# Kernel tuning notes

Measured on AMD Instinct MI355X. Metric: run time of the kernel, lower is better.

The kernel has to match this reference:

```python
import jax, jax.numpy as jnp
import numpy as np

EPS = 1e-5  # BatchNorm2d default eps


def conv1x1_bn(x, w, g, b, m, v):
    # 1x1 conv (no bias) + inference BatchNorm folded to scale/shift
    y = jnp.einsum('bchw,oc->bohw', x, w)
    s = g / jnp.sqrt(v + EPS)
    return y * s[None, :, None, None] + (b - m * s)[None, :, None, None]


def setup_inputs() -> dict:
    key = jax.random.key(0)
    ks = jax.random.split(key, 18)
    B, C, H, W = 4, 256, 64, 64
    KD, NH = 16, 8
    DH = KD * NH
    f = jax.random.normal
    u = jax.random.uniform
    return {
        'x': f(ks[0], (B, C, H, W), jnp.float32),
        'key_v_input_reduction': f(ks[1], (1,), jnp.float32),
        'w_qk': f(ks[2], (KD, C), jnp.float32) * 0.05,
        'g_qk': u(ks[3], (KD,), jnp.float32, 0.5, 1.5),
        'b_qk': f(ks[4], (KD,), jnp.float32) * 0.05,
        'm_qk': f(ks[5], (KD,), jnp.float32) * 0.05,
        'v_qk': u(ks[6], (KD,), jnp.float32, 0.5, 1.5),
        'w_v': f(ks[7], (DH, C), jnp.float32) * 0.05,
        'g_v': u(ks[8], (DH,), jnp.float32, 0.5, 1.5),
        'b_v': f(ks[9], (DH,), jnp.float32) * 0.05,
        'm_v': f(ks[10], (DH,), jnp.float32) * 0.05,
        'v_v': u(ks[11], (DH,), jnp.float32, 0.5, 1.5),
        'w_p': f(ks[12], (C, DH), jnp.float32) * 0.05,
        'g_p': u(ks[13], (C,), jnp.float32, 0.5, 1.5),
        'b_p': f(ks[14], (C,), jnp.float32) * 0.05,
        'm_p': f(ks[15], (C,), jnp.float32) * 0.05,
        'v_p': u(ks[16], (C,), jnp.float32, 0.5, 1.5),
    }


def reference(x, key_v_input_reduction, w_qk, g_qk, b_qk, m_qk, v_qk,
              w_v, g_v, b_v, m_v, v_v, w_p, g_p, b_p, m_p, v_p):
    B, C, H, W = x.shape
    N = H * W
    kd = w_qk.shape[0]
    dh = w_v.shape[0]
    nh = dh // kd
    # shared single KV head: qq == kk (share_kv=True, one_kv_head=True)
    qk = conv1x1_bn(x, w_qk, g_qk, b_qk, m_qk, v_qk).reshape(B, 1, kd, N)
    qq = jnp.swapaxes(qk, -1, -2)                      # [B,1,N,kd]
    attn = jax.nn.softmax(jnp.matmul(qq, qk), axis=-1)  # [B,1,N,N]
    vv = conv1x1_bn(x, w_v, g_v, b_v, m_v, v_v).reshape(B, nh, kd, N)
    vv = jnp.swapaxes(vv, -1, -2)                      # [B,nh,N,kd]
    xx = jnp.matmul(attn, vv)                          # broadcast head dim -> [B,nh,N,kd]
    xx = jnp.swapaxes(xx, -1, -2).reshape(B, dh, H, W)
    out = conv1x1_bn(jax.nn.relu(xx), w_p, g_p, b_p, m_p, v_p)
    return out
```

## Files before the change

kernel.cpp:

```cpp
#include <hip/hip_runtime.h>
#include <cstdint>
#include <cstddef>


typedef __attribute__((ext_vector_type(4)))  float f32x4;
typedef __attribute__((ext_vector_type(16))) float f32x16;
typedef __attribute__((ext_vector_type(8)))  _Float16 half8;
typedef __attribute__((ext_vector_type(8)))  unsigned short ushort8;
typedef __attribute__((ext_vector_type(2)))  unsigned u32x2;
typedef __attribute__((ext_vector_type(4)))  unsigned u32x4;

#define N_SP 4096
#define CIN  256
#define KDIM 16
#define DHV  128

__device__ __forceinline__ unsigned short f2h(float f) {
    _Float16 h = (_Float16)f;
    return __builtin_bit_cast(unsigned short, h);
}
__device__ __forceinline__ float h2f(unsigned short u) {
    return (float)__builtin_bit_cast(_Float16, u);
}
__device__ __forceinline__ unsigned pk2(float a, float b) {
    return (unsigned)f2h(a) | ((unsigned)f2h(b) << 16);
}
__device__ __forceinline__ unsigned shfl32u(unsigned v, int src) {
    return (unsigned)__shfl((int)v, src, 64);
}
__device__ __forceinline__ f32x4 mfma16(ushort8 a, ushort8 b, f32x4 c) {
    return __builtin_amdgcn_mfma_f32_16x16x32_f16(
        __builtin_bit_cast(half8, a), __builtin_bit_cast(half8, b), c, 0, 0, 0);
}
__device__ __forceinline__ f32x16 mfma32(half8 a, half8 b, f32x16 c) {
    return __builtin_amdgcn_mfma_f32_32x32x16_f16(a, b, c, 0, 0, 0);
}

__global__ __launch_bounds__(256) void fold_weights(
    const float* __restrict__ w_qk, const float* __restrict__ g_qk,
    const float* __restrict__ b_qk, const float* __restrict__ m_qk,
    const float* __restrict__ v_qk,
    const float* __restrict__ w_v, const float* __restrict__ g_v,
    const float* __restrict__ b_v, const float* __restrict__ m_v,
    const float* __restrict__ v_v,
    const float* __restrict__ w_p, const float* __restrict__ g_p,
    const float* __restrict__ b_p, const float* __restrict__ m_p,
    const float* __restrict__ v_p,
    unsigned short* __restrict__ wf1, float* __restrict__ shift1,
    unsigned short* __restrict__ wpf, float* __restrict__ shiftp)
{
    int row = blockIdx.x;
    int t   = threadIdx.x;
    if (row < 144) {
        float s, sh; const float* src;
        if (row < KDIM) {
            s  = g_qk[row] * rsqrtf(v_qk[row] + 1e-5f);
            sh = b_qk[row] - m_qk[row] * s;
            src = w_qk + row * CIN;
        } else {
            int o = row - KDIM;
            s  = g_v[o] * rsqrtf(v_v[o] + 1e-5f);
            sh = b_v[o] - m_v[o] * s;
            src = w_v + o * CIN;
        }
        wf1[row * CIN + t] = f2h(src[t] * s);
        if (t == 0) shift1[row] = sh;
    } else {
        int o = row - 144;
        float s = g_p[o] * rsqrtf(v_p[o] + 1e-5f);
        if (t < DHV) wpf[o * DHV + t] = f2h(w_p[o * DHV + t] * s);
        if (t == 0) shiftp[o] = b_p[o] - m_p[o] * s;
    }
}

__global__ __launch_bounds__(256) void proj_qkv(
    const float* __restrict__ x,
    const unsigned short* __restrict__ wf1, const float* __restrict__ shift1,
    unsigned short* __restrict__ qkT, unsigned short* __restrict__ Vt)
{
    const int b  = blockIdx.y;
    const int n0 = blockIdx.x * 64;
    const int tid  = threadIdx.x;
    const int w    = tid >> 6;
    const int lane = tid & 63;
    const int lg   = lane >> 4;
    const int lr   = lane & 15;
    const int n    = n0 + w * 16 + lr;

    const float* xb = x + (size_t)b * CIN * N_SP;
    f32x4 acc[9];
#pragma unroll
    for (int i = 0; i < 9; ++i) acc[i] = (f32x4){0.f, 0.f, 0.f, 0.f};

    for (int ks = 0; ks < 8; ++ks) {
        const int cbase = ks * 32 + lg * 8;
        ushort8 bx;
#pragma unroll
        for (int j = 0; j < 8; ++j) {
            float xv = xb[(size_t)(cbase + j) * N_SP + n];
            bx[j] = f2h(xv);
        }
#pragma unroll
        for (int ot = 0; ot < 9; ++ot) {
            ushort8 a = *(const ushort8*)(wf1 + (ot * 16 + lr) * CIN + cbase);
            acc[ot] = mfma16(a, bx, acc[ot]);
        }
    }

#pragma unroll
    for (int ot = 0; ot < 9; ++ot)
#pragma unroll
        for (int r = 0; r < 4; ++r) {
            int o = ot * 16 + lg * 4 + r;
            float val = acc[ot][r] + shift1[o];
            unsigned short hv = f2h(val);
            if (o < KDIM) qkT[((size_t)b * N_SP + n) * 16 + o] = hv;
            else          Vt[((size_t)b * DHV + (o - KDIM)) * N_SP + n] = hv;
        }
}

__device__ __forceinline__ void stage_v(
    const unsigned short* __restrict__ vt_b,
    unsigned short* v_l, int k0, int p, int lane)
{
#pragma unroll
    for (int s = 0; s < 8; ++s) {
        const int vi = p * 8 + s;
        const int d  = vi * 8 + (lane >> 3);
        const int c8 = (lane & 7) ^ ((lane >> 3) & 7);
        const unsigned short* src = vt_b + (size_t)d * N_SP + k0 + c8 * 8;
        __builtin_amdgcn_global_load_lds(
            (const __attribute__((address_space(1))) void*)src,
            (__attribute__((address_space(3))) void*)(v_l + vi * 512),
            16, 0, 0);
    }
}

__device__ __forceinline__ half8 ldv(const unsigned short* vl, int nb, int kc,
                                     int la31, int hi)
{
    const int d = nb * 32 + la31;
    const ushort8 v = *(const ushort8*)
        (vl + d * 64 + (((kc * 2 + hi) ^ (d & 7)) << 3));
    return __builtin_bit_cast(half8, v);
}

__device__ __forceinline__ half8 ldk(const unsigned short* qk_b, int krow,
                                     int la31, int hi)
{
    return __builtin_bit_cast(half8,
        *(const ushort8*)(qk_b + (size_t)(krow + la31) * 16 + hi * 8));
}

__global__ __launch_bounds__(512, 2) void attn_kernel(
    const unsigned short* __restrict__ qkT,
    const unsigned short* __restrict__ Vt,
    unsigned short* __restrict__ xx)
{
    const int b  = blockIdx.y;
    const int q0 = blockIdx.x * 64;
    const int tid  = threadIdx.x;
    const int ws   = tid >> 6;
    const int strm = ws >> 1;
    const int p    = ws & 1;
    const int lane = tid & 63;
    const int la31 = lane & 31;
    const int hi   = lane >> 5;

    const unsigned short* qk_b = qkT + (size_t)b * N_SP * 16;
    const unsigned short* vt_b = Vt  + (size_t)b * DHV * N_SP;
    const int kbase = strm * (N_SP / 4);
    const int qrow  = q0 + p * 32;

    const half8 aq = __builtin_bit_cast(half8,
        *(const ushort8*)(qk_b + (size_t)(qrow + la31) * 16 + hi * 8));

    f32x16 acc0, acc1, acc2, acc3, z16;
#pragma unroll
    for (int i = 0; i < 16; ++i) { z16[i] = 0.f; }
    acc0 = z16; acc1 = z16; acc2 = z16; acc3 = z16;
    float m_r = -__builtin_inff();
    float l_r = 0.f;

    __shared__ __align__(16) unsigned short v_lds[4][2][128 * 64];
    __shared__ float lmbuf[4][64][2];

    stage_v(vt_b, &v_lds[strm][0][0], kbase, p, lane);
    half8 kf0n = ldk(qk_b, kbase, la31, hi);
    half8 kf1n = ldk(qk_b, kbase + 32, la31, hi);

    for (int t = 0; t < 16; ++t) {
        const int cur = t & 1;
        __syncthreads();
        if (t < 15)
            stage_v(vt_b, &v_lds[strm][cur ^ 1][0], kbase + (t + 1) * 64,
                    p, lane);
        const half8 kf0 = kf0n;
        const half8 kf1 = kf1n;
        if (t < 15) {
            kf0n = ldk(qk_b, kbase + (t + 1) * 64, la31, hi);
            kf1n = ldk(qk_b, kbase + (t + 1) * 64 + 32, la31, hi);
        }
        const unsigned short* vl = &v_lds[strm][cur][0];

        f32x16 s0 = mfma32(kf0, aq, z16);
        f32x16 s1 = mfma32(kf1, aq, z16);

        float mpair[8];
#pragma unroll
        for (int i = 0; i < 8; ++i)
            mpair[i] = fmaxf(fmaxf(s0[i], s0[i + 8]), fmaxf(s1[i], s1[i + 8]));
        float mx = fmaxf(fmaxf(fmaxf(mpair[0], mpair[1]), fmaxf(mpair[2], mpair[3])),
                         fmaxf(fmaxf(mpair[4], mpair[5]), fmaxf(mpair[6], mpair[7])));
        mx = fmaxf(mx, __shfl(mx, lane ^ 32));

        if (!__all(mx <= m_r + 8.0f)) {
            float mnew = fmaxf(m_r, mx);
            float sc = __expf(m_r - mnew);
            l_r *= sc;
#pragma unroll
            for (int i = 0; i < 16; ++i) {
                acc0[i] *= sc; acc1[i] *= sc; acc2[i] *= sc; acc3[i] *= sc;
            }
            m_r = mnew;
        }
#pragma unroll
        for (int i = 0; i < 16; ++i) s0[i] = __expf(s0[i] - m_r);
#pragma unroll
        for (int i = 0; i < 16; ++i) s1[i] = __expf(s1[i] - m_r);
        float rpair[8];
#pragma unroll
        for (int i = 0; i < 8; ++i)
            rpair[i] = (s0[i] + s0[i + 8]) + (s1[i] + s1[i + 8]);
        l_r += ((rpair[0] + rpair[1]) + (rpair[2] + rpair[3]))
             + ((rpair[4] + rpair[5]) + (rpair[6] + rpair[7]));

#define PV_CHUNK(SV, B0, KC)                                               \
        {                                                                  \
            unsigned a0 = pk2(SV[B0 + 0], SV[B0 + 1]);                     \
            unsigned a1 = pk2(SV[B0 + 2], SV[B0 + 3]);                     \
            unsigned a2 = pk2(SV[B0 + 4], SV[B0 + 5]);                     \
            unsigned a3 = pk2(SV[B0 + 6], SV[B0 + 7]);                     \
            unsigned p0 = shfl32u(a0, lane ^ 32);                          \
            unsigned p1 = shfl32u(a1, lane ^ 32);                          \
            unsigned p2 = shfl32u(a2, lane ^ 32);                          \
            unsigned p3 = shfl32u(a3, lane ^ 32);                          \
            u32x4 pw;                                                      \
            pw.x = hi ? p2 : a0;                                           \
            pw.y = hi ? p3 : a1;                                           \
            pw.z = hi ? a2 : p0;                                           \
            pw.w = hi ? a3 : p1;                                           \
            half8 pb = __builtin_bit_cast(half8, pw);                      \
            acc0 = mfma32(ldv(vl, 0, KC, la31, hi), pb, acc0);             \
            acc1 = mfma32(ldv(vl, 1, KC, la31, hi), pb, acc1);             \
            acc2 = mfma32(ldv(vl, 2, KC, la31, hi), pb, acc2);             \
            acc3 = mfma32(ldv(vl, 3, KC, la31, hi), pb, acc3);             \
        }
        PV_CHUNK(s0, 0, 0)
        PV_CHUNK(s0, 8, 1)
        PV_CHUNK(s1, 0, 2)
        PV_CHUNK(s1, 8, 3)
#undef PV_CHUNK
    }

    l_r = l_r + __shfl(l_r, lane ^ 32);

    __syncthreads();

    unsigned short* Opart = &v_lds[0][0][0];
    const int qib = p * 32 + la31;
    if (hi == 0) {
        lmbuf[strm][qib][0] = m_r;
        lmbuf[strm][qib][1] = l_r;
    }
    {
        const float invl = 1.0f / l_r;
        const size_t qoff = ((size_t)strm * 64 + qib) * 128;
#define PUB(ACC, NB)                                                       \
        {                                                                  \
            _Pragma("unroll")                                              \
            for (int rq = 0; rq < 4; ++rq) {                               \
                float v0 = ACC[rq * 4 + 0] * invl;                         \
                float v1 = ACC[rq * 4 + 1] * invl;                         \
                float v2 = ACC[rq * 4 + 2] * invl;                         \
                float v3 = ACC[rq * 4 + 3] * invl;                         \
                u32x2 wv; wv.x = pk2(v0, v1); wv.y = pk2(v2, v3);          \
                *(u32x2*)(Opart + qoff + NB * 32 + rq * 8 + 4 * hi) = wv;  \
            }                                                              \
        }
        PUB(acc0, 0) PUB(acc1, 1) PUB(acc2, 2) PUB(acc3, 3)
#undef PUB
    }
    __syncthreads();

    {
        const int q    = tid >> 3;
        const int dseg = (tid & 7) * 16;
        const float m0 = lmbuf[0][q][0], l0 = lmbuf[0][q][1];
        const float m1 = lmbuf[1][q][0], l1 = lmbuf[1][q][1];
        const float m2 = lmbuf[2][q][0], l2 = lmbuf[2][q][1];
        const float m3 = lmbuf[3][q][0], l3 = lmbuf[3][q][1];
        const float M = fmaxf(fmaxf(m0, m1), fmaxf(m2, m3));
        float w0 = l0 * __expf(m0 - M);
        float w1 = l1 * __expf(m1 - M);
        float w2 = l2 * __expf(m2 - M);
        float w3 = l3 * __expf(m3 - M);
        const float inv = 1.0f / (w0 + w1 + w2 + w3);
        w0 *= inv; w1 *= inv; w2 *= inv; w3 *= inv;

        const ushort8 A0 = *(const ushort8*)(Opart + (0 * 64 + q) * 128 + dseg);
        const ushort8 A1 = *(const ushort8*)(Opart + (1 * 64 + q) * 128 + dseg);
        const ushort8 A2 = *(const ushort8*)(Opart + (2 * 64 + q) * 128 + dseg);
        const ushort8 A3 = *(const ushort8*)(Opart + (3 * 64 + q) * 128 + dseg);
        const ushort8 B0 = *(const ushort8*)(Opart + (0 * 64 + q) * 128 + dseg + 8);
        const ushort8 B1 = *(const ushort8*)(Opart + (1 * 64 + q) * 128 + dseg + 8);
        const ushort8 B2 = *(const ushort8*)(Opart + (2 * 64 + q) * 128 + dseg + 8);
        const ushort8 B3 = *(const ushort8*)(Opart + (3 * 64 + q) * 128 + dseg + 8);

        ushort8 o0, o1;
#pragma unroll
        for (int i = 0; i < 8; ++i) {
            float va = w0 * h2f(A0[i]) + w1 * h2f(A1[i])
                     + w2 * h2f(A2[i]) + w3 * h2f(A3[i]);
            float vb = w0 * h2f(B0[i]) + w1 * h2f(B1[i])
                     + w2 * h2f(B2[i]) + w3 * h2f(B3[i]);
            o0[i] = f2h(fmaxf(va, 0.f));
            o1[i] = f2h(fmaxf(vb, 0.f));
        }
        const size_t xo = ((size_t)b * N_SP + q0 + q) * 128 + dseg;
        *(ushort8*)(xx + xo)     = o0;
        *(ushort8*)(xx + xo + 8) = o1;
    }
}

__global__ __launch_bounds__(256) void proj_out(
    const unsigned short* __restrict__ xx,
    const unsigned short* __restrict__ wpf, const float* __restrict__ shiftp,
    float* __restrict__ out)
{
    const int b  = blockIdx.z;
    const int n0 = blockIdx.y * 64;
    const int o0 = blockIdx.x * 64 + (threadIdx.x >> 6) * 16;
    const int lane = threadIdx.x & 63;
    const int lg   = lane >> 4;
    const int lr   = lane & 15;

    f32x4 acc[4];
#pragma unroll
    for (int i = 0; i < 4; ++i) acc[i] = (f32x4){0.f, 0.f, 0.f, 0.f};

    const unsigned short* xb = xx + (size_t)b * N_SP * DHV;

    for (int ks = 0; ks < 4; ++ks) {
        ushort8 a = *(const ushort8*)(wpf + (size_t)(o0 + lr) * DHV + ks * 32 + lg * 8);
#pragma unroll
        for (int nt = 0; nt < 4; ++nt) {
            ushort8 bfr = *(const ushort8*)
                (xb + (size_t)(n0 + nt * 16 + lr) * DHV + ks * 32 + lg * 8);
            acc[nt] = mfma16(a, bfr, acc[nt]);
        }
    }

#pragma unroll
    for (int nt = 0; nt < 4; ++nt)
#pragma unroll
        for (int r = 0; r < 4; ++r) {
            int o = o0 + lg * 4 + r;
            out[((size_t)b * CIN + o) * N_SP + n0 + nt * 16 + lr]
                = acc[nt][r] + shiftp[o];
        }
}

extern "C" void kernel_launch(void* const* d_in, const int* in_sizes, int n_in,
                              void* d_out, int out_size, void* d_ws, size_t ws_size,
                              hipStream_t stream)
{
    const float* x    = (const float*)d_in[0];
    const float* w_qk = (const float*)d_in[2];
    const float* g_qk = (const float*)d_in[3];
    const float* b_qk = (const float*)d_in[4];
    const float* m_qk = (const float*)d_in[5];
    const float* v_qk = (const float*)d_in[6];
    const float* w_v  = (const float*)d_in[7];
    const float* g_v  = (const float*)d_in[8];
    const float* b_v  = (const float*)d_in[9];
    const float* m_v  = (const float*)d_in[10];
    const float* v_v  = (const float*)d_in[11];
    const float* w_p  = (const float*)d_in[12];
    const float* g_p  = (const float*)d_in[13];
    const float* b_p  = (const float*)d_in[14];
    const float* m_p  = (const float*)d_in[15];
    const float* v_p  = (const float*)d_in[16];

    char* ws = (char*)d_ws;
    unsigned short* qkT = (unsigned short*)(ws);
    unsigned short* Vt  = (unsigned short*)(ws + (1u << 20));
    unsigned short* xxb = (unsigned short*)(ws + (5u << 20));
    unsigned short* wf1 = (unsigned short*)(ws + (9u << 20));
    float* shift1       = (float*)(ws + (9u << 20) + 80 * 1024);
    unsigned short* wpf = (unsigned short*)(ws + (9u << 20) + 84 * 1024);
    float* shiftp       = (float*)(ws + (9u << 20) + 148 * 1024);

    fold_weights<<<400, 256, 0, stream>>>(
        w_qk, g_qk, b_qk, m_qk, v_qk,
        w_v, g_v, b_v, m_v, v_v,
        w_p, g_p, b_p, m_p, v_p,
        wf1, shift1, wpf, shiftp);

    proj_qkv<<<dim3(64, 4), 256, 0, stream>>>(x, wf1, shift1, qkT, Vt);

    attn_kernel<<<dim3(64, 4), 512, 0, stream>>>(qkT, Vt, xxb);

    proj_out<<<dim3(4, 64, 4), 256, 0, stream>>>(xxb, wpf, shiftp, (float*)d_out);
}
```

Measured before the change: 71.99 us.

## Fuse output projection into attention kernel, use exp2 softmax, split QKV projection waves

The output 1x1 conv+BN is now computed at the end of the attention kernel. The normalized relu'd tile is staged in LDS (reusing the V buffer) and multiplied by the folded projection weights with MFMA, which removes the xx global round trip and one kernel launch. The QK projection is pre-scaled by sqrt(log2 e) so the softmax can use exp2 directly, with the rescale threshold adjusted to match. proj_qkv now uses 512 threads, splitting the 9 output tiles across two wave groups so each thread holds fewer accumulators. In exchange, x is read twice per block in proj_qkv and the attention epilogue becomes longer.

```diff
diff --git a/kernel.cpp b/kernel.cpp
--- a/kernel.cpp
+++ b/kernel.cpp
@@ -49,6 +49,7 @@
     unsigned short* __restrict__ wf1, float* __restrict__ shift1,
     unsigned short* __restrict__ wpf, float* __restrict__ shiftp)
 {
+    const float SQL2E = 1.2011224087864498f;
     int row = blockIdx.x;
     int t   = threadIdx.x;
     if (row < 144) {
@@ -56,6 +57,7 @@
         if (row < KDIM) {
             s  = g_qk[row] * rsqrtf(v_qk[row] + 1e-5f);
             sh = b_qk[row] - m_qk[row] * s;
+            s *= SQL2E; sh *= SQL2E;
             src = w_qk + row * CIN;
         } else {
             int o = row - KDIM;
@@ -73,7 +75,7 @@
     }
 }
 
-__global__ __launch_bounds__(256) void proj_qkv(
+__global__ __launch_bounds__(512) void proj_qkv(
     const float* __restrict__ x,
     const unsigned short* __restrict__ wf1, const float* __restrict__ shift1,
     unsigned short* __restrict__ qkT, unsigned short* __restrict__ Vt)
@@ -82,41 +84,66 @@
     const int n0 = blockIdx.x * 64;
     const int tid  = threadIdx.x;
     const int w    = tid >> 6;
+    const int half = w >> 2;
+    const int wq   = w & 3;
     const int lane = tid & 63;
     const int lg   = lane >> 4;
     const int lr   = lane & 15;
-    const int n    = n0 + w * 16 + lr;
+    const int n    = n0 + wq * 16 + lr;
 
     const float* xb = x + (size_t)b * CIN * N_SP;
-    f32x4 acc[9];
-#pragma unroll
-    for (int i = 0; i < 9; ++i) acc[i] = (f32x4){0.f, 0.f, 0.f, 0.f};
-
-    for (int ks = 0; ks < 8; ++ks) {
-        const int cbase = ks * 32 + lg * 8;
-        ushort8 bx;
-#pragma unroll
-        for (int j = 0; j < 8; ++j) {
-            float xv = xb[(size_t)(cbase + j) * N_SP + n];
-            bx[j] = f2h(xv);
-        }
-#pragma unroll
-        for (int ot = 0; ot < 9; ++ot) {
-            ushort8 a = *(const ushort8*)(wf1 + (ot * 16 + lr) * CIN + cbase);
-            acc[ot] = mfma16(a, bx, acc[ot]);
-        }
-    }
-
-#pragma unroll
-    for (int ot = 0; ot < 9; ++ot)
-#pragma unroll
-        for (int r = 0; r < 4; ++r) {
-            int o = ot * 16 + lg * 4 + r;
-            float val = acc[ot][r] + shift1[o];
-            unsigned short hv = f2h(val);
-            if (o < KDIM) qkT[((size_t)b * N_SP + n) * 16 + o] = hv;
-            else          Vt[((size_t)b * DHV + (o - KDIM)) * N_SP + n] = hv;
-        }
+
+    if (half == 0) {
+        f32x4 acc[5];
+#pragma unroll
+        for (int i = 0; i < 5; ++i) acc[i] = (f32x4){0.f, 0.f, 0.f, 0.f};
+        for (int ks = 0; ks < 8; ++ks) {
+            const int cbase = ks * 32 + lg * 8;
+            ushort8 bx;
+#pragma unroll
+            for (int j = 0; j < 8; ++j)
+                bx[j] = f2h(xb[(size_t)(cbase + j) * N_SP + n]);
+#pragma unroll
+            for (int i = 0; i < 5; ++i) {
+                ushort8 a = *(const ushort8*)(wf1 + (i * 16 + lr) * CIN + cbase);
+                acc[i] = mfma16(a, bx, acc[i]);
+            }
+        }
+#pragma unroll
+        for (int i = 0; i < 5; ++i)
+#pragma unroll
+            for (int r = 0; r < 4; ++r) {
+                int o = i * 16 + lg * 4 + r;
+                float val = acc[i][r] + shift1[o];
+                unsigned short hv = f2h(val);
+                if (o < KDIM) qkT[((size_t)b * N_SP + n) * 16 + o] = hv;
+                else          Vt[((size_t)b * DHV + (o - KDIM)) * N_SP + n] = hv;
+            }
+    } else {
+        f32x4 acc[4];
+#pragma unroll
+        for (int i = 0; i < 4; ++i) acc[i] = (f32x4){0.f, 0.f, 0.f, 0.f};
+        for (int ks = 0; ks < 8; ++ks) {
+            const int cbase = ks * 32 + lg * 8;
+            ushort8 bx;
+#pragma unroll
+            for (int j = 0; j < 8; ++j)
+                bx[j] = f2h(xb[(size_t)(cbase + j) * N_SP + n]);
+#pragma unroll
+            for (int i = 0; i < 4; ++i) {
+                ushort8 a = *(const ushort8*)(wf1 + ((i + 5) * 16 + lr) * CIN + cbase);
+                acc[i] = mfma16(a, bx, acc[i]);
+            }
+        }
+#pragma unroll
+        for (int i = 0; i < 4; ++i)
+#pragma unroll
+            for (int r = 0; r < 4; ++r) {
+                int o = (i + 5) * 16 + lg * 4 + r;
+                float val = acc[i][r] + shift1[o];
+                Vt[((size_t)b * DHV + (o - KDIM)) * N_SP + n] = f2h(val);
+            }
+    }
 }
 
 __device__ __forceinline__ void stage_v(
@@ -155,7 +182,9 @@
 __global__ __launch_bounds__(512, 2) void attn_kernel(
     const unsigned short* __restrict__ qkT,
     const unsigned short* __restrict__ Vt,
-    unsigned short* __restrict__ xx)
+    const unsigned short* __restrict__ wpf,
+    const float* __restrict__ shiftp,
+    float* __restrict__ out)
 {
     const int b  = blockIdx.y;
     const int q0 = blockIdx.x * 64;
@@ -214,9 +243,9 @@
                          fmaxf(fmaxf(mpair[4], mpair[5]), fmaxf(mpair[6], mpair[7])));
         mx = fmaxf(mx, __shfl(mx, lane ^ 32));
 
-        if (!__all(mx <= m_r + 8.0f)) {
+        if (!__all(mx <= m_r + 11.54f)) {
             float mnew = fmaxf(m_r, mx);
-            float sc = __expf(m_r - mnew);
+            float sc = exp2f(m_r - mnew);
             l_r *= sc;
 #pragma unroll
             for (int i = 0; i < 16; ++i) {
@@ -225,9 +254,9 @@
             m_r = mnew;
         }
 #pragma unroll
-        for (int i = 0; i < 16; ++i) s0[i] = __expf(s0[i] - m_r);
-#pragma unroll
-        for (int i = 0; i < 16; ++i) s1[i] = __expf(s1[i] - m_r);
+        for (int i = 0; i < 16; ++i) s0[i] = exp2f(s0[i] - m_r);
+#pragma unroll
+        for (int i = 0; i < 16; ++i) s1[i] = exp2f(s1[i] - m_r);
         float rpair[8];
 #pragma unroll
         for (int i = 0; i < 8; ++i)
@@ -293,6 +322,7 @@
     }
     __syncthreads();
 
+    unsigned short* olds = &v_lds[2][0][0];
     {
         const int q    = tid >> 3;
         const int dseg = (tid & 7) * 16;
@@ -301,10 +331,10 @@
         const float m2 = lmbuf[2][q][0], l2 = lmbuf[2][q][1];
         const float m3 = lmbuf[3][q][0], l3 = lmbuf[3][q][1];
         const float M = fmaxf(fmaxf(m0, m1), fmaxf(m2, m3));
-        float w0 = l0 * __expf(m0 - M);
-        float w1 = l1 * __expf(m1 - M);
-        float w2 = l2 * __expf(m2 - M);
-        float w3 = l3 * __expf(m3 - M);
+        float w0 = l0 * exp2f(m0 - M);
+        float w1 = l1 * exp2f(m1 - M);
+        float w2 = l2 * exp2f(m2 - M);
+        float w3 = l3 * exp2f(m3 - M);
         const float inv = 1.0f / (w0 + w1 + w2 + w3);
         w0 *= inv; w1 *= inv; w2 *= inv; w3 *= inv;
 
@@ -327,48 +357,47 @@
             o0[i] = f2h(fmaxf(va, 0.f));
             o1[i] = f2h(fmaxf(vb, 0.f));
         }
-        const size_t xo = ((size_t)b * N_SP + q0 + q) * 128 + dseg;
-        *(ushort8*)(xx + xo)     = o0;
-        *(ushort8*)(xx + xo + 8) = o1;
-    }
-}
-
-__global__ __launch_bounds__(256) void proj_out(
-    const unsigned short* __restrict__ xx,
-    const unsigned short* __restrict__ wpf, const float* __restrict__ shiftp,
-    float* __restrict__ out)
-{
-    const int b  = blockIdx.z;
-    const int n0 = blockIdx.y * 64;
-    const int o0 = blockIdx.x * 64 + (threadIdx.x >> 6) * 16;
-    const int lane = threadIdx.x & 63;
-    const int lg   = lane >> 4;
-    const int lr   = lane & 15;
-
-    f32x4 acc[4];
-#pragma unroll
-    for (int i = 0; i < 4; ++i) acc[i] = (f32x4){0.f, 0.f, 0.f, 0.f};
-
-    const unsigned short* xb = xx + (size_t)b * N_SP * DHV;
-
-    for (int ks = 0; ks < 4; ++ks) {
-        ushort8 a = *(const ushort8*)(wpf + (size_t)(o0 + lr) * DHV + ks * 32 + lg * 8);
-#pragma unroll
-        for (int nt = 0; nt < 4; ++nt) {
-            ushort8 bfr = *(const ushort8*)
-                (xb + (size_t)(n0 + nt * 16 + lr) * DHV + ks * 32 + lg * 8);
-            acc[nt] = mfma16(a, bfr, acc[nt]);
-        }
-    }
-
-#pragma unroll
-    for (int nt = 0; nt < 4; ++nt)
-#pragma unroll
-        for (int r = 0; r < 4; ++r) {
-            int o = o0 + lg * 4 + r;
-            out[((size_t)b * CIN + o) * N_SP + n0 + nt * 16 + lr]
-                = acc[nt][r] + shiftp[o];
-        }
+        *(ushort8*)(olds + q * 136 + dseg)     = o0;
+        *(ushort8*)(olds + q * 136 + dseg + 8) = o1;
+    }
+    __syncthreads();
+
+    {
+        const int lr16 = lane & 15;
+        const int lg16 = lane >> 4;
+        const int ob   = ws * 32;
+
+        f32x4 pacc[2][4];
+#pragma unroll
+        for (int i = 0; i < 2; ++i)
+#pragma unroll
+            for (int j = 0; j < 4; ++j) pacc[i][j] = (f32x4){0.f, 0.f, 0.f, 0.f};
+
+        for (int ks = 0; ks < 4; ++ks) {
+            ushort8 a0 = *(const ushort8*)
+                (wpf + (size_t)(ob + lr16) * DHV + ks * 32 + lg16 * 8);
+            ushort8 a1 = *(const ushort8*)
+                (wpf + (size_t)(ob + 16 + lr16) * DHV + ks * 32 + lg16 * 8);
+#pragma unroll
+            for (int qt = 0; qt < 4; ++qt) {
+                ushort8 bfr = *(const ushort8*)
+                    (olds + (qt * 16 + lr16) * 136 + ks * 32 + lg16 * 8);
+                pacc[0][qt] = mfma16(a0, bfr, pacc[0][qt]);
+                pacc[1][qt] = mfma16(a1, bfr, pacc[1][qt]);
+            }
+        }
+
+#pragma unroll
+        for (int t2 = 0; t2 < 2; ++t2)
+#pragma unroll
+            for (int qt = 0; qt < 4; ++qt)
+#pragma unroll
+                for (int r = 0; r < 4; ++r) {
+                    int o = ob + t2 * 16 + lg16 * 4 + r;
+                    out[((size_t)b * CIN + o) * N_SP + q0 + qt * 16 + lr16]
+                        = pacc[t2][qt][r] + shiftp[o];
+                }
+    }
 }
 
 extern "C" void kernel_launch(void* const* d_in, const int* in_sizes, int n_in,
@@ -395,7 +424,6 @@
     char* ws = (char*)d_ws;
     unsigned short* qkT = (unsigned short*)(ws);
     unsigned short* Vt  = (unsigned short*)(ws + (1u << 20));
-    unsigned short* xxb = (unsigned short*)(ws + (5u << 20));
     unsigned short* wf1 = (unsigned short*)(ws + (9u << 20));
     float* shift1       = (float*)(ws + (9u << 20) + 80 * 1024);
     unsigned short* wpf = (unsigned short*)(ws + (9u << 20) + 84 * 1024);
@@ -407,9 +435,8 @@
         w_p, g_p, b_p, m_p, v_p,
         wf1, shift1, wpf, shiftp);
 
-    proj_qkv<<<dim3(64, 4), 256, 0, stream>>>(x, wf1, shift1, qkT, Vt);
-
-    attn_kernel<<<dim3(64, 4), 512, 0, stream>>>(qkT, Vt, xxb);
-
-    proj_out<<<dim3(4, 64, 4), 256, 0, stream>>>(xxb, wpf, shiftp, (float*)d_out);
-}
+    proj_qkv<<<dim3(64, 4), 512, 0, stream>>>(x, wf1, shift1, qkT, Vt);
+
+    attn_kernel<<<dim3(64, 4), 512, 0, stream>>>(
+        qkT, Vt, wpf, shiftp, (float*)d_out);
+}
```

New measurement: 69.94 us (median of 2 runs). -2.8%, faster.
